# Optimization experiments

Hardware: AMD Instinct MI355X
Metric: run time of the kernel (lower is better)

## Reference

```python
import jax, jax.numpy as jnp
import numpy as np

B, T = 16, 100
MCL = 100      # MAX_CODE_LEN
D_IN = 200     # input_dim (= ques_encoding)
D_BERT = 768
KC = 50        # KC_one_hot_dim
KCD = 100      # kc_embed_dim
HID = 128
SCALE_BERT = 100
TW = 0.5       # QPALA_config.total_attention_weight
BTW = 0.5      # BLAA_config.total_attention_weight


def setup_inputs():
    key = jax.random.key(0)
    ks = jax.random.split(key, 20)
    f32 = jnp.float32
    # composite input feature vector: [ques_enc | code2vec idx | bert | time | score | kc one-hot]
    rnn_first = (jax.random.uniform(ks[0], (B, T, D_IN)) < 0.1).astype(f32)
    c2v = jax.random.randint(ks[1], (B, T, 3 * MCL), 0, 10000).astype(f32)
    bert = jax.random.normal(ks[2], (B, T, D_BERT), f32)
    time_f = jax.random.uniform(ks[3], (B, T, 10), f32)
    score_f = jax.random.uniform(ks[4], (B, T, 2), f32)
    kc = (jax.random.uniform(ks[5], (B, T, KC)) < 0.15).astype(f32)
    x = jnp.concatenate([rnn_first, c2v, bert, time_f, score_f, kc], axis=2)  # [B,T,1330]
    s = 0.05
    p = lambda k, shp: jax.random.normal(k, shp, f32) * s
    return dict(
        x=x,
        node_emb=p(ks[6], (10002, 100)),
        path_emb=p(ks[7], (20002, 100)),
        Wb=p(ks[8], (SCALE_BERT, D_BERT)), bb=jnp.zeros((SCALE_BERT,), f32),
        Wna=p(ks[9], (500, 500)), bna=jnp.zeros((500,), f32),
        Wia=p(ks[10], (KCD, 500)), bia=jnp.zeros((KCD,), f32),
        Wattn=p(ks[11], (1, 500)), battn=jnp.zeros((1,), f32),
        kc_emb=p(ks[12], (KC, KCD)),
        Wt=p(ks[13], (1, SCALE_BERT + KC + KCD)), bt=jnp.zeros((1,), f32),
        Wih=p(ks[14], (4 * HID, 950)), Whh=p(ks[15], (4 * HID, HID)),
        bih=jnp.zeros((4 * HID,), f32), bhh=jnp.zeros((4 * HID,), f32),
        Wfc=p(ks[16], (100, HID + KC + D_IN)), bfc=jnp.zeros((100,), f32),
    )


def _lstm(xseq, Wih, Whh, bih, bhh):
    # PyTorch LSTM, gate order i,f,g,o; batch_first
    bsz = xseq.shape[0]
    pre = jnp.einsum('btd,gd->btg', xseq, Wih) + bih + bhh  # [B,T,4H]

    def step(carry, g_in):
        h, c = carry
        g = g_in + h @ Whh.T
        i, f, gg, o = jnp.split(g, 4, axis=-1)
        c = jax.nn.sigmoid(f) * c + jax.nn.sigmoid(i) * jnp.tanh(gg)
        h = jax.nn.sigmoid(o) * jnp.tanh(c)
        return (h, c), h

    init = (jnp.zeros((bsz, HID), xseq.dtype), jnp.zeros((bsz, HID), xseq.dtype))
    _, hs = jax.lax.scan(step, init, jnp.swapaxes(pre, 0, 1))
    return jnp.swapaxes(hs, 0, 1)


def _forward(x, node_emb, path_emb, Wb, bb, Wna, bna, Wia, bia, Wattn, battn,
             kc_emb, Wt, bt, Wih, Whh, bih, bhh, Wfc, bfc):
    b, t = x.shape[0], x.shape[1]
    rnn_first = x[:, :, :D_IN]
    bert = x[:, :, 500:500 + D_BERT]
    kc_part = x[:, :, 1280:1280 + KC]
    c2v = x[:, :, D_IN:D_IN + 3 * MCL].reshape(b, t, MCL, 3).astype(jnp.int32)
    # gather embeddings + broadcast encoding -> full_embed [B,T,MCL,500]
    full = jnp.concatenate([
        node_emb[c2v[..., 0]], node_emb[c2v[..., 2]], path_emb[c2v[..., 1]],
        jnp.broadcast_to(rnn_first[:, :, None, :], (b, t, MCL, D_IN))], axis=3)
    bert_vec = bert @ Wb.T + bb  # [B,T,100]
    # non-interactive attention pooling (NB: original softmaxes over dim=1 = time)
    cw = jnp.tanh(full @ Wna.T + bna) @ Wattn.T + battn  # [B,T,MCL,1]
    aw = jax.nn.softmax(cw, axis=1)
    na = jnp.sum(full * aw, axis=2)  # [B,T,500]
    kcn = jnp.sum(kc_part, axis=2, keepdims=True)
    kcn = jnp.where(kcn == 0, 1.0, kcn)
    # interactive (KC) cross attention
    trans = full @ Wia.T + bia  # [B,T,MCL,KCD]
    Q = kc_part[..., None] * kc_emb[None, None]  # [B,T,KC,KCD]
    attn = jax.nn.softmax(jnp.einsum('btkd,btmd->btkm', Q, trans), axis=-1)
    Hm = jnp.einsum('btkm,btmd->btkd', attn, trans) * kc_part[..., None]
    ia = jnp.sum(Hm, axis=2) / kcn  # [B,T,KCD]
    rnn_input = jnp.concatenate([kc_part, rnn_first, ia, na, bert_vec], axis=2)  # [B,T,950]
    lstm_out = _lstm(rnn_input, Wih, Whh, bih, bhh)  # [B,T,HID]
    # per-time-step causal attention over lstm_out (vectorized form of the python loop)
    w = (jnp.concatenate([bert_vec, kc_part, ia], axis=2) @ Wt.T + bt)[..., 0]  # [B,T]
    mask = jnp.tril(jnp.ones((t, t), bool))
    logits = jnp.where(mask[None], w[:, None, :], -1e30)
    cattn = jax.nn.softmax(logits, axis=-1)  # [B,T,T]
    cur = jnp.einsum('bij,bjh->bih', cattn, lstm_out)
    attended = lstm_out * (1.0 - TW)
    attended = attended.at[:, 0].set(lstm_out[:, 0])
    idx = jnp.arange(t)
    addm = ((idx >= 1) & (idx <= t - 2)).astype(x.dtype)[None, :, None]
    attended = attended + cur * BTW * addm
    out = jax.nn.sigmoid(
        jnp.concatenate([rnn_first, kc_part, attended], axis=2) @ Wfc.T + bfc)
    return out  # [B,T,100]


def reference(x, node_emb, path_emb, Wb, bb, Wna, bna, Wia, bia, Wattn, battn,
              kc_emb, Wt, bt, Wih, Whh, bih, bhh, Wfc, bfc):
    return _forward(x, node_emb, path_emb, Wb, bb, Wna, bna, Wia, bia, Wattn, battn,
                    kc_emb, Wt, bt, Wih, Whh, bih, bhh, Wfc, bfc)
```

## Files before the change

kernel.cpp:

```cpp
#include <hip/hip_runtime.h>
#include <math.h>

typedef unsigned short ushort_t;
typedef __attribute__((ext_vector_type(8))) short bf16x8;
typedef __attribute__((ext_vector_type(4))) float f32x4;

constexpr int CB = 16, CT = 100, CMCL = 100, CDIN = 200;
constexpr int CKC = 50, CHID = 128;
constexpr int XCH = 1330;
constexpr int NBT = CB * CT;
constexpr int NNODE = 10002, NPATH = 20002;
constexpr int TRS = 114;
constexpr int HSTR = 136;
constexpr int NODE_W = 1536;
constexpr int PATH_W = 768;
constexpr int XR_W   = 640;

__device__ __forceinline__ float frcp(float v){ return __builtin_amdgcn_rcpf(v); }
__device__ __forceinline__ float fsigmoid(float v){ return frcp(1.f + __expf(-v)); }
__device__ __forceinline__ float ftanh_(float v){
  float e = __expf(-2.f*fabsf(v));
  return copysignf((1.f - e) * frcp(1.f + e), v);
}
__device__ __forceinline__ float wredsum(float v){
  #pragma unroll
  for (int off = 32; off; off >>= 1) v += __shfl_xor(v, off);
  return v;
}
__device__ __forceinline__ float wredmax(float v){
  #pragma unroll
  for (int off = 32; off; off >>= 1) v = fmaxf(v, __shfl_xor(v, off));
  return v;
}
__device__ __forceinline__ ushort_t f2b(float f){
  union { float f; unsigned u; } c{f};
  return (ushort_t)((c.u + 0x7FFFu + ((c.u >> 16) & 1u)) >> 16);
}
__device__ __forceinline__ float b2f(unsigned hbits){
  union { unsigned u; float f; } c{hbits << 16};
  return c.f;
}
__device__ __forceinline__ void b8f(const ushort_t* p, float* o){
  uint4 v = *reinterpret_cast<const uint4*>(p);
  o[0]=b2f(v.x & 0xFFFFu); o[1]=b2f(v.x >> 16);
  o[2]=b2f(v.y & 0xFFFFu); o[3]=b2f(v.y >> 16);
  o[4]=b2f(v.z & 0xFFFFu); o[5]=b2f(v.z >> 16);
  o[6]=b2f(v.w & 0xFFFFu); o[7]=b2f(v.w >> 16);
}

struct GDesc {
  const float* A; const float* B; float* Cf; ushort_t* Cb;
  int lda, kOff, kMax, K, M, Npad, rbp, cb, nsplit, ldc, blocks;
};
struct MegaArgs { GDesc d[4]; int nd; };

__global__ __launch_bounds__(256) void mega_gemm(MegaArgs args)
{
  constexpr int KS = 136;
  __shared__ ushort_t As[128*KS];
  __shared__ ushort_t Bs[128*KS];
  int id = blockIdx.x;
  int di = 0;
  while (di < args.nd-1 && id >= args.d[di].blocks) { id -= args.d[di].blocks; ++di; }
  GDesc g = args.d[di];
  const int per = g.rbp * g.cb;
  const int sp = id / per, r = id % per;
  const int xcd = r & 7, s2 = r >> 3;
  const int y = xcd + 8*(s2 / g.cb), cbi = s2 % g.cb;
  const int bm = y*128, bn = cbi*128;
  if (bm >= g.M) return;
  const int tid = threadIdx.x, lane = tid & 63, w = tid >> 6;
  const int wm = w & 1, wn = w >> 1;
  const int lr = lane & 15, lkq = lane >> 4;
  const int kbase = g.kOff + sp * g.K;
  const int hK = g.K >> 1;

  for (int f = tid; f < 128*hK; f += 256) {
    int row = f / hK, j2 = (f % hK)*2;
    int gm = bm + row;
    float2 va = make_float2(0.f,0.f);
    if (gm < g.M && kbase + j2 + 2 <= g.kMax)
      va = *reinterpret_cast<const float2*>(g.A + (long)gm*g.lda + kbase + j2);
    *reinterpret_cast<unsigned*>(&As[row*KS + j2]) = (unsigned)f2b(va.x) | ((unsigned)f2b(va.y)<<16);
    float2 vb = *reinterpret_cast<const float2*>(g.B + ((long)sp*g.Npad + bn + row)*g.K + j2);
    *reinterpret_cast<unsigned*>(&Bs[row*KS + j2]) = (unsigned)f2b(vb.x) | ((unsigned)f2b(vb.y)<<16);
  }
  const int padw = (128 - g.K) >> 1;
  for (int f = tid; f < 128*padw; f += 256) {
    int row = f / padw, jd = f % padw;
    *reinterpret_cast<unsigned*>(&As[row*KS + g.K + jd*2]) = 0u;
    *reinterpret_cast<unsigned*>(&Bs[row*KS + g.K + jd*2]) = 0u;
  }
  __syncthreads();

  f32x4 acc[4][4];
  #pragma unroll
  for (int i = 0; i < 4; ++i)
    #pragma unroll
    for (int j = 0; j < 4; ++j) acc[i][j] = f32x4{0.f,0.f,0.f,0.f};
  #pragma unroll
  for (int ks = 0; ks < 4; ++ks) {
    const int ko = ks*32 + lkq*8;
    bf16x8 af[4], bf[4];
    #pragma unroll
    for (int i = 0; i < 4; ++i)
      af[i] = *reinterpret_cast<const bf16x8*>(&As[(wm*64 + i*16 + lr)*KS + ko]);
    #pragma unroll
    for (int j = 0; j < 4; ++j)
      bf[j] = *reinterpret_cast<const bf16x8*>(&Bs[(wn*64 + j*16 + lr)*KS + ko]);
    #pragma unroll
    for (int i = 0; i < 4; ++i)
      #pragma unroll
      for (int j = 0; j < 4; ++j)
        acc[i][j] = __builtin_amdgcn_mfma_f32_16x16x32_bf16(af[i], bf[j], acc[i][j], 0, 0, 0);
  }
  #pragma unroll
  for (int i = 0; i < 4; ++i) {
    #pragma unroll
    for (int j = 0; j < 4; ++j) {
      #pragma unroll
      for (int rr = 0; rr < 4; ++rr) {
        int gr = bm + wm*64 + i*16 + lkq*4 + rr;
        int gc = bn + wn*64 + j*16 + lr;
        if (gr < g.M) {
          if (g.Cb) g.Cb[(long)gr * g.ldc + gc] = f2b(acc[i][j][rr]);
          else      g.Cf[((long)sp*g.M + gr)*g.ldc + gc] = acc[i][j][rr];
        }
      }
    }
  }
}

constexpr long PK_E0 = (long)NODE_W*100;
constexpr long PK_E1 = PK_E0 + (long)PATH_W*100;
constexpr long PK_E2 = PK_E1 + 2L*XR_W*100;
constexpr long PK_E3 = PK_E2 + 6L*128*128;
constexpr long PK_E4 = PK_E3 + 10L*512*96;
constexpr long PK_E5 = PK_E4 + 512;
constexpr long PK_E6 = PK_E5 + 378L*100;

__global__ void pack_all(
    const float* __restrict__ Wna, const float* __restrict__ Wia,
    const float* __restrict__ bna, const float* __restrict__ bia,
    const float* __restrict__ Wb, const float* __restrict__ Wih,
    const float* __restrict__ Wattn, const float* __restrict__ Wfc,
    float* __restrict__ Bn, float* __restrict__ Bp,
    float* __restrict__ XB2, float* __restrict__ bias_x,
    float* __restrict__ BertB, float* __restrict__ P2B,
    ushort_t* __restrict__ WAB, float* __restrict__ WfcT)
{
  long i = (long)blockIdx.x*256 + threadIdx.x;
  if (i < PK_E0) {
    int n = (int)(i / 100), k = (int)(i % 100);
    float v = 0.f;
    if (n < 500)                      v = Wna[(long)n*500 + k];
    else if (n >= 512 && n < 1012)    v = Wna[(long)(n-512)*500 + 100 + k];
    else if (n >= 1024 && n < 1124)   v = (k == n-1024) ? 1.f : 0.f;
    else if (n >= 1136 && n < 1236)   v = Wia[(long)(n-1136)*500 + k];
    else if (n >= 1280 && n < 1380)   v = (k == n-1280) ? 1.f : 0.f;
    else if (n >= 1392 && n < 1492)   v = Wia[(long)(n-1392)*500 + 100 + k];
    Bn[i] = v;
  } else if (i < PK_E1) {
    long j = i - PK_E0;
    int n = (int)(j / 100), k = (int)(j % 100);
    float v = 0.f;
    if (n < 500)                    v = Wna[(long)n*500 + 200 + k];
    else if (n >= 512 && n < 612)   v = (k == n-512) ? 1.f : 0.f;
    else if (n >= 624 && n < 724)   v = Wia[(long)(n-624)*500 + 200 + k];
    Bp[j] = v;
  } else if (i < PK_E2) {
    long j = i - PK_E1;
    if (j < XR_W) {
      float b = 0.f;
      if (j < 500) b = bna[j];
      else if (j >= 512 && j < 612) b = bia[j-512];
      bias_x[j] = b;
    }
    int s = (int)(j / (XR_W*100)), n = (int)((j / 100) % XR_W), k = (int)(j % 100);
    int k2 = s*100 + k;
    float v = 0.f;
    if (n < 500)                  v = Wna[(long)n*500 + 300 + k2];
    else if (n >= 512 && n < 612) v = Wia[(long)(n-512)*500 + 300 + k2];
    XB2[j] = v;
  } else if (i < PK_E3) {
    long j = i - PK_E2;
    int s = (int)(j / (128*128)), n = (int)((j / 128) % 128), k = (int)(j % 128);
    BertB[j] = (n < 100) ? Wb[(long)n*768 + s*128 + k] : 0.f;
  } else if (i < PK_E4) {
    long j = i - PK_E3;
    int s = (int)(j / (512*96)), n = (int)((j / 96) % 512), k = (int)(j % 96);
    int kg = s*96 + k;
    P2B[j] = (kg < 950) ? Wih[(long)n*950 + kg] : 0.f;
  } else if (i < PK_E5) {
    long j = i - PK_E4;
    WAB[j] = (j < 500) ? f2b(Wattn[j]) : (ushort_t)0;
  } else if (i < PK_E6) {
    long j = i - PK_E5;
    int o = (int)(j / 378), q = (int)(j % 378);
    WfcT[q*100 + o] = Wfc[j];
  }
}

__global__ __launch_bounds__(256) void reduce1(
    const float* __restrict__ xrP, const float* __restrict__ bias_x, ushort_t* __restrict__ XR,
    const float* __restrict__ bertP, const float* __restrict__ bb, float* __restrict__ rnn)
{
  int bt = blockIdx.x, tid = threadIdx.x;
  for (int c = tid; c < XR_W; c += 256) {
    float v = xrP[(long)bt*XR_W + c] + xrP[((long)NBT + bt)*XR_W + c] + bias_x[c];
    XR[(long)bt*XR_W + c] = f2b(v);
  }
  if (tid < 100) {
    float v = bb[tid];
    #pragma unroll
    for (int s = 0; s < 6; ++s) v += bertP[((long)s*NBT + bt)*128 + tid];
    rnn[(long)bt*950 + 850 + tid] = v;
  }
}

__global__ __launch_bounds__(512) void reduce_p2(
    const float* __restrict__ p2P, const float* __restrict__ bih, const float* __restrict__ bhh,
    ushort_t* __restrict__ P2)
{
  int bt = blockIdx.x, g = threadIdx.x;
  float v = bih[g] + bhh[g];
  #pragma unroll
  for (int s = 0; s < 10; ++s) v += p2P[((long)s*NBT + bt)*512 + g];
  int bq = bt / CT, tt = bt % CT;
  int q = g >> 7, rem = g & 127, ww = rem >> 4, lr2 = rem & 15;
  int lk2 = bq >> 2, rr = bq & 3;
  P2[((((long)tt*4 + q)*8 + ww)*4 + lk2)*64 + lr2*4 + rr] = f2b(v);
}

__global__ __launch_bounds__(256) void cw2_kernel(
    const float* __restrict__ x, const ushort_t* __restrict__ NODE_ALL,
    const ushort_t* __restrict__ PATH_ALL, const ushort_t* __restrict__ XR,
    const ushort_t* __restrict__ WAB,
    const float* __restrict__ battn, float* __restrict__ cwT)
{
  int bt = blockIdx.x, b = bt / CT, t = bt % CT;
  int tid = threadIdx.x, w = tid >> 6, lane = tid & 63;
  __shared__ int idx_s[300];
  for (int i = tid; i < 300; i += 256) idx_s[i] = (int)x[(long)bt*XCH + 200 + i];
  float rseg[8], wseg[8];
  b8f(XR + (long)bt*XR_W + lane*8, rseg);
  b8f(WAB + lane*8, wseg);
  __syncthreads();
  float bat = battn[0];

  uint4 A0, C0, P0, A1, C1, P1;
  auto issue = [&](int m, uint4& A, uint4& C, uint4& P){
    if (m < CMCL) {
      int ai = idx_s[3*m], pi = idx_s[3*m+1], ci = idx_s[3*m+2];
      A = *reinterpret_cast<const uint4*>(NODE_ALL + (long)ai*NODE_W + lane*8);
      C = *reinterpret_cast<const uint4*>(NODE_ALL + (long)ci*NODE_W + 512 + lane*8);
      P = *reinterpret_cast<const uint4*>(PATH_ALL + (long)pi*PATH_W + lane*8);
    }
  };
  auto proc = [&](int m, const uint4& A, const uint4& C, const uint4& P){
    if (m >= CMCL) return;
    const unsigned ua[4] = {A.x, A.y, A.z, A.w};
    const unsigned uc[4] = {C.x, C.y, C.z, C.w};
    const unsigned up[4] = {P.x, P.y, P.z, P.w};
    float acc = 0.f;
    #pragma unroll
    for (int jj = 0; jj < 4; ++jj) {
      float lo = b2f(ua[jj] & 0xffffu) + b2f(uc[jj] & 0xffffu) + b2f(up[jj] & 0xffffu) + rseg[2*jj];
      float hi = b2f(ua[jj] >> 16)     + b2f(uc[jj] >> 16)     + b2f(up[jj] >> 16)     + rseg[2*jj+1];
      acc = fmaf(ftanh_(lo), wseg[2*jj], acc);
      acc = fmaf(ftanh_(hi), wseg[2*jj+1], acc);
    }
    acc = wredsum(acc);
    if (lane == 0) cwT[((long)b*CMCL + m)*CT + t] = acc + bat;
  };

  issue(w, A0, C0, P0);
  for (int it = 0; it < 25; it += 2) {
    int m0 = w + it*4;
    issue(m0 + 4, A1, C1, P1);
    proc(m0, A0, C0, P0);
    issue(m0 + 8, A0, C0, P0);
    proc(m0 + 4, A1, C1, P1);
  }
}

__global__ void aw_kernel(const float* __restrict__ cwT, float* __restrict__ awT)
{
  int bm = blockIdx.x; int lane = threadIdx.x;
  const float* row = cwT + (long)bm * CT;
  bool h1 = lane < (CT - 64);
  float v0 = row[lane];
  float v1 = h1 ? row[64 + lane] : -3.0e38f;
  float mx = wredmax(fmaxf(v0, v1));
  float e0 = __expf(v0 - mx);
  float e1 = h1 ? __expf(v1 - mx) : 0.f;
  float s = wredsum(e0 + e1);
  float inv = frcp(s);
  awT[(long)bm*CT + lane] = e0 * inv;
  if (h1) awT[(long)bm*CT + 64 + lane] = e1 * inv;
}

__global__ __launch_bounds__(256) void fuse2_kernel(
    const float* __restrict__ x,
    const ushort_t* __restrict__ NODE_ALL, const ushort_t* __restrict__ PATH_ALL,
    const ushort_t* __restrict__ XR, const float* __restrict__ awT,
    const float* __restrict__ kc_emb, float* __restrict__ rnn,
    const float* __restrict__ Wt, const float* __restrict__ bt0, float* __restrict__ wbuf)
{
  int bt = blockIdx.x, b = bt / CT, t = bt % CT;
  int tid = threadIdx.x, w = tid >> 6, lane = tid & 63;
  int sub = lane >> 5, li = lane & 31;

  __shared__ ushort_t tr_s[100*TRS];
  __shared__ float nacc[4][344];
  __shared__ float ia_red[4][104];
  __shared__ float ia_f[100];
  __shared__ float aw_s[100];
  __shared__ int   idx_s[300];
  __shared__ float kcl[CKC];
  __shared__ int   act_k[CKC];
  __shared__ int   nact_s;
  __shared__ float kcn_s, awsum_s;

  for (int i = tid; i < 300; i += 256) idx_s[i] = (int)x[(long)bt*XCH + 200 + i];
  if (tid < 100) aw_s[tid] = awT[((long)b*CMCL + tid)*CT + t];
  if (tid < CKC) kcl[tid] = x[(long)bt*XCH + 1280 + tid];
  __syncthreads();
  if (tid == 0) {
    float kcn = 0.f; int na = 0;
    for (int k = 0; k < CKC; ++k) { float v = kcl[k]; kcn += v; if (v != 0.f) act_k[na++] = k; }
    nact_s = na; kcn_s = (kcn == 0.f) ? 1.f : kcn;
    float s = 0.f;
    for (int m = 0; m < CMCL; ++m) s += aw_s[m];
    awsum_s = s;
  }
  float rwseg[8];
  if (li >= 14 && li < 28) b8f(XR + (long)bt*XR_W + 512 + (li-14)*8, rwseg);
  __syncthreads();

  float na_a[8] = {}, na_c[8] = {}, na_p[8] = {};
  uint4 A0, C0, P0, A1, C1, P1;
  auto g_issue = [&](int m, uint4& A, uint4& C, uint4& P){
    if (m < CMCL) {
      int ai = idx_s[3*m], pi = idx_s[3*m+1], ci = idx_s[3*m+2];
      A = *reinterpret_cast<const uint4*>(NODE_ALL + (long)ai*NODE_W + 1024 + li*8);
      C = *reinterpret_cast<const uint4*>(NODE_ALL + (long)ci*NODE_W + 1280 + li*8);
      P = *reinterpret_cast<const uint4*>(PATH_ALL + (long)pi*PATH_W + 512  + li*8);
    }
  };
  auto g_proc = [&](int m, const uint4& A, const uint4& C, const uint4& P){
    if (m >= CMCL || li >= 28) return;
    const unsigned ua[4] = {A.x, A.y, A.z, A.w};
    const unsigned uc[4] = {C.x, C.y, C.z, C.w};
    const unsigned up[4] = {P.x, P.y, P.z, P.w};
    if (li < 14) {
      float awm = aw_s[m];
      #pragma unroll
      for (int jj = 0; jj < 4; ++jj) {
        na_a[2*jj]   = fmaf(awm, b2f(ua[jj] & 0xffffu), na_a[2*jj]);
        na_a[2*jj+1] = fmaf(awm, b2f(ua[jj] >> 16),     na_a[2*jj+1]);
        na_c[2*jj]   = fmaf(awm, b2f(uc[jj] & 0xffffu), na_c[2*jj]);
        na_c[2*jj+1] = fmaf(awm, b2f(uc[jj] >> 16),     na_c[2*jj+1]);
        na_p[2*jj]   = fmaf(awm, b2f(up[jj] & 0xffffu), na_p[2*jj]);
        na_p[2*jj+1] = fmaf(awm, b2f(up[jj] >> 16),     na_p[2*jj+1]);
      }
    } else {
      unsigned* d32 = reinterpret_cast<unsigned*>(&tr_s[m*TRS + (li-14)*8]);
      #pragma unroll
      for (int jj = 0; jj < 4; ++jj) {
        float lo = b2f(ua[jj] & 0xffffu) + b2f(uc[jj] & 0xffffu) + b2f(up[jj] & 0xffffu) + rwseg[2*jj];
        float hi = b2f(ua[jj] >> 16)     + b2f(uc[jj] >> 16)     + b2f(up[jj] >> 16)     + rwseg[2*jj+1];
        d32[jj] = (unsigned)f2b(lo) | ((unsigned)f2b(hi) << 16);
      }
    }
  };
  const int mb = w*2 + sub;
  g_issue(mb, A0, C0, P0);
  for (int it = 0; it < 13; it += 2) {
    g_issue((it+1)*8 + mb, A1, C1, P1);
    g_proc(it*8 + mb, A0, C0, P0);
    g_issue((it+2)*8 + mb, A0, C0, P0);
    g_proc((it+1)*8 + mb, A1, C1, P1);
  }
  #pragma unroll
  for (int j = 0; j < 8; ++j) {
    na_a[j] += __shfl_xor(na_a[j], 32);
    na_c[j] += __shfl_xor(na_c[j], 32);
    na_p[j] += __shfl_xor(na_p[j], 32);
  }
  if (lane < 14) {
    #pragma unroll
    for (int j = 0; j < 8; ++j) {
      nacc[w][      lane*8 + j] = na_a[j];
      nacc[w][112 + lane*8 + j] = na_c[j];
      nacc[w][224 + lane*8 + j] = na_p[j];
    }
  }
  __syncthreads();

  for (int q = tid; q < 336; q += 256) {
    float v = nacc[0][q] + nacc[1][q] + nacc[2][q] + nacc[3][q];
    int seg = q / 112, col = q % 112;
    if (col < 100) rnn[(long)bt*950 + 350 + seg*100 + col] = v;
  }
  for (int q = tid; q < CDIN; q += 256) {
    float xv = x[(long)bt*XCH + q];
    rnn[(long)bt*950 + 50 + q] = xv;
    rnn[(long)bt*950 + 650 + q] = awsum_s * xv;
  }
  if (tid < CKC) rnn[(long)bt*950 + tid] = kcl[tid];

  float ia0 = 0.f, ia1 = 0.f;
  const bool vrow1 = lane < 36;
  const bool vpv   = lane < 50;
  const int nact = nact_s;
  const unsigned* tr32_0 = reinterpret_cast<const unsigned*>(&tr_s[lane*TRS]);
  const unsigned* tr32_1 = reinterpret_cast<const unsigned*>(&tr_s[(64+lane)*TRS]);
  const unsigned* tr32   = reinterpret_cast<const unsigned*>(tr_s);
  for (int ki = w; ki < nact; ki += 4) {
    int k = act_k[ki];
    float kck = kcl[k];
    const float* ke = kc_emb + (long)k*100;
    float s0 = 0.f, s1 = 0.f;
    #pragma unroll 5
    for (int dh = 0; dh < 50; ++dh) {
      float k0 = ke[2*dh], k1 = ke[2*dh+1];
      unsigned u0 = tr32_0[dh];
      s0 = fmaf(k0, b2f(u0 & 0xffffu), s0);
      s0 = fmaf(k1, b2f(u0 >> 16), s0);
      if (vrow1) {
        unsigned u1 = tr32_1[dh];
        s1 = fmaf(k0, b2f(u1 & 0xffffu), s1);
        s1 = fmaf(k1, b2f(u1 >> 16), s1);
      }
    }
    s0 *= kck; s1 *= kck;
    float mx = wredmax(fmaxf(s0, vrow1 ? s1 : -3.0e38f));
    float p0e = __expf(s0 - mx);
    float p1e = vrow1 ? __expf(s1 - mx) : 0.f;
    float sm = wredsum(p0e + p1e);
    float inv = kck * frcp(sm);
    p0e *= inv; p1e *= inv;
    #pragma unroll 4
    for (int m = 0; m < CMCL; ++m) {
      float pm = (m < 64) ? __shfl(p0e, m) : __shfl(p1e, m - 64);
      if (vpv) {
        unsigned u = tr32[m*57 + lane];
        ia0 = fmaf(pm, b2f(u & 0xffffu), ia0);
        ia1 = fmaf(pm, b2f(u >> 16), ia1);
      }
    }
  }
  if (vpv) { ia_red[w][2*lane] = ia0; ia_red[w][2*lane+1] = ia1; }
  __syncthreads();
  if (tid < 100) {
    float v = (ia_red[0][tid] + ia_red[1][tid] + ia_red[2][tid] + ia_red[3][tid]) * frcp(kcn_s);
    rnn[(long)bt*950 + 250 + tid] = v;
    ia_f[tid] = v;
  }
  __syncthreads();
  if (tid < 64) {
    float acc = 0.f;
    for (int i = tid; i < 250; i += 64) {
      float f;
      if (i < 100)      f = rnn[(long)bt*950 + 850 + i];
      else if (i < 150) f = kcl[i - 100];
      else              f = ia_f[i - 150];
      acc = fmaf(Wt[i], f, acc);
    }
    acc = wredsum(acc);
    if (tid == 0) wbuf[bt] = acc + bt0[0];
  }
}

__global__ __launch_bounds__(512) void lstm_mfma2(
    const ushort_t* __restrict__ P2,
    const float* __restrict__ Whh,
    float* __restrict__ lstm_out)
{
  const int tid = threadIdx.x, lane = tid & 63, w = tid >> 6;
  const int lr = lane & 15, lkq = lane >> 4;
  __shared__ ushort_t H[2][16 * HSTR];
  {
    ushort_t* hp = &H[0][0];
    for (int i = tid; i < 2*16*HSTR; i += 512) hp[i] = 0;
  }

  bf16x8 bw0[4], bw1[4], bw2[4], bw3[4];
  #pragma unroll
  for (int kk = 0; kk < 4; ++kk) {
    short s[8];
    const float* wp0 = Whh + (long)(0*128 + w*16 + lr) * 128 + kk*32 + lkq*8;
    const float* wp1 = Whh + (long)(1*128 + w*16 + lr) * 128 + kk*32 + lkq*8;
    const float* wp2 = Whh + (long)(2*128 + w*16 + lr) * 128 + kk*32 + lkq*8;
    const float* wp3 = Whh + (long)(3*128 + w*16 + lr) * 128 + kk*32 + lkq*8;
    #pragma unroll
    for (int j = 0; j < 8; ++j) s[j] = (short)f2b(wp0[j]);
    bw0[kk] = bf16x8{s[0],s[1],s[2],s[3],s[4],s[5],s[6],s[7]};
    #pragma unroll
    for (int j = 0; j < 8; ++j) s[j] = (short)f2b(wp1[j]);
    bw1[kk] = bf16x8{s[0],s[1],s[2],s[3],s[4],s[5],s[6],s[7]};
    #pragma unroll
    for (int j = 0; j < 8; ++j) s[j] = (short)f2b(wp2[j]);
    bw2[kk] = bf16x8{s[0],s[1],s[2],s[3],s[4],s[5],s[6],s[7]};
    #pragma unroll
    for (int j = 0; j < 8; ++j) s[j] = (short)f2b(wp3[j]);
    bw3[kk] = bf16x8{s[0],s[1],s[2],s[3],s[4],s[5],s[6],s[7]};
  }

  auto pptr = [&](int t, int q){
    return reinterpret_cast<const uint2*>(P2 + (((((long)t*4 + q)*8 + w)*4 + lkq)*64 + lr*4));
  };
  uint2 pc0 = *pptr(0,0), pc1 = *pptr(0,1), pc2 = *pptr(0,2), pc3 = *pptr(0,3);
  uint2 pn0, pn1, pn2, pn3;
  f32x4 c = {0.f,0.f,0.f,0.f};
  __syncthreads();

  int pb = 0;
  for (int t = 0; t < CT; ++t) {
    if (t + 1 < CT) { pn0 = *pptr(t+1,0); pn1 = *pptr(t+1,1); pn2 = *pptr(t+1,2); pn3 = *pptr(t+1,3); }
    bf16x8 a[4];
    #pragma unroll
    for (int kk = 0; kk < 4; ++kk)
      a[kk] = *reinterpret_cast<const bf16x8*>(&H[pb][lr*HSTR + kk*32 + lkq*8]);
    f32x4 acc0 = f32x4{ b2f(pc0.x & 0xffffu), b2f(pc0.x >> 16), b2f(pc0.y & 0xffffu), b2f(pc0.y >> 16) };
    f32x4 acc1 = f32x4{ b2f(pc1.x & 0xffffu), b2f(pc1.x >> 16), b2f(pc1.y & 0xffffu), b2f(pc1.y >> 16) };
    f32x4 acc2 = f32x4{ b2f(pc2.x & 0xffffu), b2f(pc2.x >> 16), b2f(pc2.y & 0xffffu), b2f(pc2.y >> 16) };
    f32x4 acc3 = f32x4{ b2f(pc3.x & 0xffffu), b2f(pc3.x >> 16), b2f(pc3.y & 0xffffu), b2f(pc3.y >> 16) };
    #pragma unroll
    for (int kk = 0; kk < 4; ++kk) {
      acc0 = __builtin_amdgcn_mfma_f32_16x16x32_bf16(a[kk], bw0[kk], acc0, 0,0,0);
      acc1 = __builtin_amdgcn_mfma_f32_16x16x32_bf16(a[kk], bw1[kk], acc1, 0,0,0);
      acc2 = __builtin_amdgcn_mfma_f32_16x16x32_bf16(a[kk], bw2[kk], acc2, 0,0,0);
      acc3 = __builtin_amdgcn_mfma_f32_16x16x32_bf16(a[kk], bw3[kk], acc3, 0,0,0);
    }
    #pragma unroll
    for (int r = 0; r < 4; ++r) {
      float ig = fsigmoid(acc0[r]);
      float fg = fsigmoid(acc1[r]);
      float gg = ftanh_(acc2[r]);
      float og = fsigmoid(acc3[r]);
      c[r] = fg*c[r] + ig*gg;
      float h = og * ftanh_(c[r]);
      int row = lkq*4 + r;
      H[pb^1][row*HSTR + w*16 + lr] = f2b(h);
      lstm_out[((long)row*CT + t)*128 + w*16 + lr] = h;
    }
    __syncthreads();
    pb ^= 1;
    pc0 = pn0; pc1 = pn1; pc2 = pn2; pc3 = pn3;
  }
}

__global__ __launch_bounds__(256) void final_kernel(
    const float* __restrict__ x, const float* __restrict__ wbuf,
    const float* __restrict__ lstm_out, const float* __restrict__ WfcT,
    const float* __restrict__ bfc, float* __restrict__ out)
{
  int bt = blockIdx.x; int b = bt / CT, i = bt % CT;
  int tid = threadIdx.x;
  __shared__ float p_s[CT];
  __shared__ float feat_s[384];
  if (tid < 64) {
    bool h1 = (64 + tid) < CT;
    float v0 = (tid <= i) ? wbuf[(long)b*CT + tid] : -3.0e38f;
    float v1 = (h1 && (64 + tid) <= i) ? wbuf[(long)b*CT + 64 + tid] : -3.0e38f;
    float mx = wredmax(fmaxf(v0, v1));
    float e0 = (tid <= i) ? __expf(v0 - mx) : 0.f;
    float e1 = (h1 && (64 + tid) <= i) ? __expf(v1 - mx) : 0.f;
    float s = wredsum(e0 + e1);
    float inv = frcp(s);
    p_s[tid] = e0 * inv;
    if (h1) p_s[64 + tid] = e1 * inv;
  }
  __syncthreads();
  if (tid < CHID) {
    float cur = 0.f;
    #pragma unroll 4
    for (int j = 0; j <= i; ++j) cur = fmaf(p_s[j], lstm_out[((long)b*CT + j)*CHID + tid], cur);
    float l = lstm_out[((long)b*CT + i)*CHID + tid];
    float att;
    if (i == 0) att = l;
    else { att = 0.5f * l; if (i <= CT - 2) att = fmaf(0.5f, cur, att); }
    feat_s[250 + tid] = att;
  }
  for (int q = tid; q < 250; q += 256)
    feat_s[q] = (q < 200) ? x[(long)bt*XCH + q] : x[(long)bt*XCH + 1280 + (q - 200)];
  __syncthreads();
  if (tid < 100) {
    float acc = bfc[tid];
    #pragma unroll 4
    for (int q = 0; q < 378; ++q) acc = fmaf(WfcT[q*100 + tid], feat_s[q], acc);
    out[(long)bt*100 + tid] = fsigmoid(acc);
  }
}

extern "C" void kernel_launch(void* const* d_in, const int* in_sizes, int n_in,
                              void* d_out, int out_size, void* d_ws, size_t ws_size,
                              hipStream_t stream) {
  (void)in_sizes; (void)n_in; (void)out_size; (void)ws_size;
  const float* x        = (const float*)d_in[0];
  const float* node_emb = (const float*)d_in[1];
  const float* path_emb = (const float*)d_in[2];
  const float* Wb       = (const float*)d_in[3];
  const float* bb       = (const float*)d_in[4];
  const float* Wna      = (const float*)d_in[5];
  const float* bna      = (const float*)d_in[6];
  const float* Wia      = (const float*)d_in[7];
  const float* bia      = (const float*)d_in[8];
  const float* Wattn    = (const float*)d_in[9];
  const float* battn    = (const float*)d_in[10];
  const float* kc_emb   = (const float*)d_in[11];
  const float* Wt       = (const float*)d_in[12];
  const float* bt0      = (const float*)d_in[13];
  const float* Wih      = (const float*)d_in[14];
  const float* Whh      = (const float*)d_in[15];
  const float* bih      = (const float*)d_in[16];
  const float* bhh      = (const float*)d_in[17];
  const float* Wfc      = (const float*)d_in[18];
  const float* bfc      = (const float*)d_in[19];
  float* out = (float*)d_out;

  char* cur = (char*)d_ws;
  auto alloc = [&](size_t bytes)->char* {
    char* p = cur; cur += (bytes + 255) & ~(size_t)255; return p;
  };
  ushort_t* NODE_ALL = (ushort_t*)alloc((size_t)NNODE*NODE_W*2);
  ushort_t* PATH_ALL = (ushort_t*)alloc((size_t)NPATH*PATH_W*2);
  ushort_t* XR   = (ushort_t*)alloc((size_t)NBT*XR_W*2);
  float* Bn     = (float*)alloc((size_t)NODE_W*100*4);
  float* Bp     = (float*)alloc((size_t)PATH_W*100*4);
  float* XB2    = (float*)alloc((size_t)2*XR_W*100*4);
  float* BertB  = (float*)alloc((size_t)6*128*128*4);
  float* P2B    = (float*)alloc((size_t)10*512*96*4);
  float* bias_x = (float*)alloc((size_t)XR_W*4);
  ushort_t* WAB = (ushort_t*)alloc(512*2);
  float* cwT  = (float*)alloc((size_t)NBT*100*4);
  float* awT  = (float*)alloc((size_t)NBT*100*4);
  float* rnn  = (float*)alloc((size_t)NBT*950*4);
  char*  uni  = alloc((size_t)10*NBT*512*4);
  float* xrP   = (float*)uni;
  float* bertP = (float*)(uni + (size_t)2*NBT*XR_W*4);
  float* p2P   = (float*)uni;
  ushort_t* P2 = (ushort_t*)alloc((size_t)NBT*512*2);
  float* lstm = (float*)alloc((size_t)NBT*128*4);
  float* wbuf = (float*)alloc((size_t)NBT*4);
  float* WfcT = (float*)alloc((size_t)378*100*4);

  pack_all<<<(unsigned)((PK_E6 + 255)/256), 256, 0, stream>>>(
      Wna, Wia, bna, bia, Wb, Wih, Wattn, Wfc,
      Bn, Bp, XB2, bias_x, BertB, P2B, WAB, WfcT);

  {
    MegaArgs a{};
    a.nd = 4;
    a.d[0] = { node_emb, Bn, nullptr, NODE_ALL, 100, 0, 100, 100, NNODE, NODE_W, 80, 12, 1, NODE_W, 80*12 };
    a.d[1] = { path_emb, Bp, nullptr, PATH_ALL, 100, 0, 100, 100, NPATH, PATH_W, 160, 6, 1, PATH_W, 160*6 };
    a.d[2] = { x, BertB, bertP, nullptr, XCH, 500, 1268, 128, NBT, 128, 16, 1, 6, 128, 16*1*6 };
    a.d[3] = { x, XB2, xrP, nullptr, XCH, 0, 200, 100, NBT, XR_W, 16, 5, 2, XR_W, 16*5*2 };
    int total = a.d[0].blocks + a.d[1].blocks + a.d[2].blocks + a.d[3].blocks;
    mega_gemm<<<total, 256, 0, stream>>>(a);
  }
  reduce1<<<NBT, 256, 0, stream>>>(xrP, bias_x, XR, bertP, bb, rnn);

  cw2_kernel<<<NBT,256,0,stream>>>(x, NODE_ALL, PATH_ALL, XR, WAB, battn, cwT);
  aw_kernel<<<CB*CMCL,64,0,stream>>>(cwT, awT);
  fuse2_kernel<<<NBT,256,0,stream>>>(x, NODE_ALL, PATH_ALL, XR, awT, kc_emb, rnn, Wt, bt0, wbuf);

  {
    MegaArgs a{};
    a.nd = 1;
    a.d[0] = { rnn, P2B, p2P, nullptr, 950, 0, 950, 96, NBT, 512, 16, 4, 10, 512, 16*4*10 };
    mega_gemm<<<a.d[0].blocks, 256, 0, stream>>>(a);
  }
  reduce_p2<<<NBT, 512, 0, stream>>>(p2P, bih, bhh, P2);

  lstm_mfma2<<<1,512,0,stream>>>(P2, Whh, lstm);
  final_kernel<<<NBT,256,0,stream>>>(x, wbuf, lstm, WfcT, bfc, out);
}
```

Measured before the change: 485.7 us.

## Store attention-path projected embeddings in custom FP8 and widen fuse2 to 512 threads

Splits the projected node/path embedding tables into an 8-bit (software e4m3-like) table used by the attention-score kernel and a bf16 table used by the fusion kernel. The XR row projection is split the same way. This halves the gather bytes in cw2_kernel at the cost of extra decode ALU work and lower precision inside the tanh attention logits. fuse2_kernel moves to 512 threads with 8 warps sharing the per-code gather loop and reductions, to add parallelism.

```diff
diff --git a/kernel.cpp b/kernel.cpp
--- a/kernel.cpp
+++ b/kernel.cpp
@@ -2,6 +2,7 @@
 #include <math.h>
 
 typedef unsigned short ushort_t;
+typedef unsigned char uchar_t;
 typedef __attribute__((ext_vector_type(8))) short bf16x8;
 typedef __attribute__((ext_vector_type(4))) float f32x4;
 
@@ -12,9 +13,11 @@
 constexpr int NNODE = 10002, NPATH = 20002;
 constexpr int TRS = 114;
 constexpr int HSTR = 136;
-constexpr int NODE_W = 1536;
-constexpr int PATH_W = 768;
-constexpr int XR_W   = 640;
+constexpr int NT8_W = 1024;
+constexpr int NTB_W = 512;
+constexpr int PT8_W = 512;
+constexpr int PTB_W = 256;
+constexpr int XR_W  = 640;
 
 __device__ __forceinline__ float frcp(float v){ return __builtin_amdgcn_rcpf(v); }
 __device__ __forceinline__ float fsigmoid(float v){ return frcp(1.f + __expf(-v)); }
@@ -47,12 +50,41 @@
   o[4]=b2f(v.z & 0xFFFFu); o[5]=b2f(v.z >> 16);
   o[6]=b2f(v.w & 0xFFFFu); o[7]=b2f(v.w >> 16);
 }
+__device__ __forceinline__ uchar_t ff8(float f){
+  union { float f; unsigned u; } c{f};
+  unsigned s = (c.u >> 24) & 0x80u;
+  c.u &= 0x7FFFFFFFu;
+  float a = c.f;
+  unsigned b;
+  if (a < 0.015625f) {
+    b = (unsigned)(a * 512.f + 0.5f);
+  } else {
+    unsigned u = c.u + (0x0007FFFFu + ((c.u >> 20) & 1u));
+    int e = (int)(u >> 23) - 120;
+    unsigned mm = (u >> 20) & 7u;
+    if (e >= 16) { e = 15; mm = 6; }
+    b = ((unsigned)e << 3) | mm;
+  }
+  return (uchar_t)(s | b);
+}
+__device__ __forceinline__ float f8d(unsigned b){
+  unsigned e = (b >> 3) & 15u, m = b & 7u;
+  union { unsigned u; float f; } c{((e + 120u) << 23) | (m << 20)};
+  float v = e ? c.f : (float)m * 0.001953125f;
+  return (b & 0x80u) ? -v : v;
+}
+__device__ __forceinline__ void f8x8(uint2 p, float* o){
+  #pragma unroll
+  for (int j = 0; j < 4; ++j) o[j]     = f8d((p.x >> (8*j)) & 255u);
+  #pragma unroll
+  for (int j = 0; j < 4; ++j) o[4 + j] = f8d((p.y >> (8*j)) & 255u);
+}
 
 struct GDesc {
-  const float* A; const float* B; float* Cf; ushort_t* Cb;
-  int lda, kOff, kMax, K, M, Npad, rbp, cb, nsplit, ldc, blocks;
+  const float* A; const float* B; float* Cf; void* Cb;
+  int lda, kOff, kMax, K, M, Npad, rbp, cb, nsplit, ldc, omode, blocks;
 };
-struct MegaArgs { GDesc d[4]; int nd; };
+struct MegaArgs { GDesc d[6]; int nd; };
 
 __global__ __launch_bounds__(256) void mega_gemm(MegaArgs args)
 {
@@ -123,28 +155,33 @@
         int gr = bm + wm*64 + i*16 + lkq*4 + rr;
         int gc = bn + wn*64 + j*16 + lr;
         if (gr < g.M) {
-          if (g.Cb) g.Cb[(long)gr * g.ldc + gc] = f2b(acc[i][j][rr]);
-          else      g.Cf[((long)sp*g.M + gr)*g.ldc + gc] = acc[i][j][rr];
+          float v = acc[i][j][rr];
+          if (g.omode == 2)      ((uchar_t*)g.Cb)[(long)gr * g.ldc + gc] = ff8(v);
+          else if (g.omode == 1) ((ushort_t*)g.Cb)[(long)gr * g.ldc + gc] = f2b(v);
+          else                   g.Cf[((long)sp*g.M + gr)*g.ldc + gc] = v;
         }
       }
     }
   }
 }
 
-constexpr long PK_E0 = (long)NODE_W*100;
-constexpr long PK_E1 = PK_E0 + (long)PATH_W*100;
-constexpr long PK_E2 = PK_E1 + 2L*XR_W*100;
-constexpr long PK_E3 = PK_E2 + 6L*128*128;
-constexpr long PK_E4 = PK_E3 + 10L*512*96;
-constexpr long PK_E5 = PK_E4 + 512;
-constexpr long PK_E6 = PK_E5 + 378L*100;
+constexpr long PK_E0 = 1024L*100;
+constexpr long PK_E1 = PK_E0 + 512L*100;
+constexpr long PK_E2 = PK_E1 + 512L*100;
+constexpr long PK_E3 = PK_E2 + 256L*100;
+constexpr long PK_E4 = PK_E3 + 2L*XR_W*100;
+constexpr long PK_E5 = PK_E4 + 6L*128*128;
+constexpr long PK_E6 = PK_E5 + 10L*512*96;
+constexpr long PK_E7 = PK_E6 + 512;
+constexpr long PK_E8 = PK_E7 + 378L*100;
 
 __global__ void pack_all(
     const float* __restrict__ Wna, const float* __restrict__ Wia,
     const float* __restrict__ bna, const float* __restrict__ bia,
     const float* __restrict__ Wb, const float* __restrict__ Wih,
     const float* __restrict__ Wattn, const float* __restrict__ Wfc,
-    float* __restrict__ Bn, float* __restrict__ Bp,
+    float* __restrict__ Bn8, float* __restrict__ Bnb,
+    float* __restrict__ Bp8, float* __restrict__ Bpb,
     float* __restrict__ XB2, float* __restrict__ bias_x,
     float* __restrict__ BertB, float* __restrict__ P2B,
     ushort_t* __restrict__ WAB, float* __restrict__ WfcT)
@@ -153,23 +190,31 @@
   if (i < PK_E0) {
     int n = (int)(i / 100), k = (int)(i % 100);
     float v = 0.f;
-    if (n < 500)                      v = Wna[(long)n*500 + k];
-    else if (n >= 512 && n < 1012)    v = Wna[(long)(n-512)*500 + 100 + k];
-    else if (n >= 1024 && n < 1124)   v = (k == n-1024) ? 1.f : 0.f;
-    else if (n >= 1136 && n < 1236)   v = Wia[(long)(n-1136)*500 + k];
-    else if (n >= 1280 && n < 1380)   v = (k == n-1280) ? 1.f : 0.f;
-    else if (n >= 1392 && n < 1492)   v = Wia[(long)(n-1392)*500 + 100 + k];
-    Bn[i] = v;
+    if (n < 500)                    v = Wna[(long)n*500 + k];
+    else if (n >= 512 && n < 1012)  v = Wna[(long)(n-512)*500 + 100 + k];
+    Bn8[i] = v;
   } else if (i < PK_E1) {
     long j = i - PK_E0;
     int n = (int)(j / 100), k = (int)(j % 100);
     float v = 0.f;
-    if (n < 500)                    v = Wna[(long)n*500 + 200 + k];
-    else if (n >= 512 && n < 612)   v = (k == n-512) ? 1.f : 0.f;
-    else if (n >= 624 && n < 724)   v = Wia[(long)(n-624)*500 + 200 + k];
-    Bp[j] = v;
+    if (n < 100)                    v = (k == n) ? 1.f : 0.f;
+    else if (n >= 112 && n < 212)   v = Wia[(long)(n-112)*500 + k];
+    else if (n >= 256 && n < 356)   v = (k == n-256) ? 1.f : 0.f;
+    else if (n >= 368 && n < 468)   v = Wia[(long)(n-368)*500 + 100 + k];
+    Bnb[j] = v;
   } else if (i < PK_E2) {
     long j = i - PK_E1;
+    int n = (int)(j / 100), k = (int)(j % 100);
+    Bp8[j] = (n < 500) ? Wna[(long)n*500 + 200 + k] : 0.f;
+  } else if (i < PK_E3) {
+    long j = i - PK_E2;
+    int n = (int)(j / 100), k = (int)(j % 100);
+    float v = 0.f;
+    if (n < 100)                    v = (k == n) ? 1.f : 0.f;
+    else if (n >= 112 && n < 212)   v = Wia[(long)(n-112)*500 + 200 + k];
+    Bpb[j] = v;
+  } else if (i < PK_E4) {
+    long j = i - PK_E3;
     if (j < XR_W) {
       float b = 0.f;
       if (j < 500) b = bna[j];
@@ -182,33 +227,35 @@
     if (n < 500)                  v = Wna[(long)n*500 + 300 + k2];
     else if (n >= 512 && n < 612) v = Wia[(long)(n-512)*500 + 300 + k2];
     XB2[j] = v;
-  } else if (i < PK_E3) {
-    long j = i - PK_E2;
+  } else if (i < PK_E5) {
+    long j = i - PK_E4;
     int s = (int)(j / (128*128)), n = (int)((j / 128) % 128), k = (int)(j % 128);
     BertB[j] = (n < 100) ? Wb[(long)n*768 + s*128 + k] : 0.f;
-  } else if (i < PK_E4) {
-    long j = i - PK_E3;
+  } else if (i < PK_E6) {
+    long j = i - PK_E5;
     int s = (int)(j / (512*96)), n = (int)((j / 96) % 512), k = (int)(j % 96);
     int kg = s*96 + k;
     P2B[j] = (kg < 950) ? Wih[(long)n*950 + kg] : 0.f;
-  } else if (i < PK_E5) {
-    long j = i - PK_E4;
+  } else if (i < PK_E7) {
+    long j = i - PK_E6;
     WAB[j] = (j < 500) ? f2b(Wattn[j]) : (ushort_t)0;
-  } else if (i < PK_E6) {
-    long j = i - PK_E5;
+  } else if (i < PK_E8) {
+    long j = i - PK_E7;
     int o = (int)(j / 378), q = (int)(j % 378);
     WfcT[q*100 + o] = Wfc[j];
   }
 }
 
 __global__ __launch_bounds__(256) void reduce1(
-    const float* __restrict__ xrP, const float* __restrict__ bias_x, ushort_t* __restrict__ XR,
+    const float* __restrict__ xrP, const float* __restrict__ bias_x,
+    uchar_t* __restrict__ XRF8, ushort_t* __restrict__ XRBF,
     const float* __restrict__ bertP, const float* __restrict__ bb, float* __restrict__ rnn)
 {
   int bt = blockIdx.x, tid = threadIdx.x;
   for (int c = tid; c < XR_W; c += 256) {
     float v = xrP[(long)bt*XR_W + c] + xrP[((long)NBT + bt)*XR_W + c] + bias_x[c];
-    XR[(long)bt*XR_W + c] = f2b(v);
+    if (c < 512) XRF8[(long)bt*512 + c] = ff8(v);
+    else         XRBF[(long)bt*128 + (c - 512)] = f2b(v);
   }
   if (tid < 100) {
     float v = bb[tid];
@@ -233,8 +280,8 @@
 }
 
 __global__ __launch_bounds__(256) void cw2_kernel(
-    const float* __restrict__ x, const ushort_t* __restrict__ NODE_ALL,
-    const ushort_t* __restrict__ PATH_ALL, const ushort_t* __restrict__ XR,
+    const float* __restrict__ x, const uchar_t* __restrict__ NT8,
+    const uchar_t* __restrict__ PT8, const uchar_t* __restrict__ XRF8,
     const ushort_t* __restrict__ WAB,
     const float* __restrict__ battn, float* __restrict__ cwT)
 {
@@ -243,33 +290,28 @@
   __shared__ int idx_s[300];
   for (int i = tid; i < 300; i += 256) idx_s[i] = (int)x[(long)bt*XCH + 200 + i];
   float rseg[8], wseg[8];
-  b8f(XR + (long)bt*XR_W + lane*8, rseg);
+  f8x8(*reinterpret_cast<const uint2*>(XRF8 + (long)bt*512 + lane*8), rseg);
   b8f(WAB + lane*8, wseg);
   __syncthreads();
   float bat = battn[0];
 
-  uint4 A0, C0, P0, A1, C1, P1;
-  auto issue = [&](int m, uint4& A, uint4& C, uint4& P){
+  uint2 A0, C0, P0, A1, C1, P1;
+  auto issue = [&](int m, uint2& A, uint2& C, uint2& P){
     if (m < CMCL) {
       int ai = idx_s[3*m], pi = idx_s[3*m+1], ci = idx_s[3*m+2];
-      A = *reinterpret_cast<const uint4*>(NODE_ALL + (long)ai*NODE_W + lane*8);
-      C = *reinterpret_cast<const uint4*>(NODE_ALL + (long)ci*NODE_W + 512 + lane*8);
-      P = *reinterpret_cast<const uint4*>(PATH_ALL + (long)pi*PATH_W + lane*8);
+      A = *reinterpret_cast<const uint2*>(NT8 + (long)ai*NT8_W + lane*8);
+      C = *reinterpret_cast<const uint2*>(NT8 + (long)ci*NT8_W + 512 + lane*8);
+      P = *reinterpret_cast<const uint2*>(PT8 + (long)pi*PT8_W + lane*8);
     }
   };
-  auto proc = [&](int m, const uint4& A, const uint4& C, const uint4& P){
+  auto proc = [&](int m, const uint2& A, const uint2& C, const uint2& P){
     if (m >= CMCL) return;
-    const unsigned ua[4] = {A.x, A.y, A.z, A.w};
-    const unsigned uc[4] = {C.x, C.y, C.z, C.w};
-    const unsigned up[4] = {P.x, P.y, P.z, P.w};
+    float fa[8], fc[8], fp[8];
+    f8x8(A, fa); f8x8(C, fc); f8x8(P, fp);
     float acc = 0.f;
     #pragma unroll
-    for (int jj = 0; jj < 4; ++jj) {
-      float lo = b2f(ua[jj] & 0xffffu) + b2f(uc[jj] & 0xffffu) + b2f(up[jj] & 0xffffu) + rseg[2*jj];
-      float hi = b2f(ua[jj] >> 16)     + b2f(uc[jj] >> 16)     + b2f(up[jj] >> 16)     + rseg[2*jj+1];
-      acc = fmaf(ftanh_(lo), wseg[2*jj], acc);
-      acc = fmaf(ftanh_(hi), wseg[2*jj+1], acc);
-    }
+    for (int j = 0; j < 8; ++j)
+      acc = fmaf(ftanh_(fa[j] + fc[j] + fp[j] + rseg[j]), wseg[j], acc);
     acc = wredsum(acc);
     if (lane == 0) cwT[((long)b*CMCL + m)*CT + t] = acc + bat;
   };
@@ -300,10 +342,10 @@
   if (h1) awT[(long)bm*CT + 64 + lane] = e1 * inv;
 }
 
-__global__ __launch_bounds__(256) void fuse2_kernel(
+__global__ __launch_bounds__(512) void fuse2_kernel(
     const float* __restrict__ x,
-    const ushort_t* __restrict__ NODE_ALL, const ushort_t* __restrict__ PATH_ALL,
-    const ushort_t* __restrict__ XR, const float* __restrict__ awT,
+    const ushort_t* __restrict__ NTB, const ushort_t* __restrict__ PTB,
+    const ushort_t* __restrict__ XRBF, const float* __restrict__ awT,
     const float* __restrict__ kc_emb, float* __restrict__ rnn,
     const float* __restrict__ Wt, const float* __restrict__ bt0, float* __restrict__ wbuf)
 {
@@ -312,8 +354,8 @@
   int sub = lane >> 5, li = lane & 31;
 
   __shared__ ushort_t tr_s[100*TRS];
-  __shared__ float nacc[4][344];
-  __shared__ float ia_red[4][104];
+  __shared__ float nacc[8][344];
+  __shared__ float ia_red[8][104];
   __shared__ float ia_f[100];
   __shared__ float aw_s[100];
   __shared__ int   idx_s[300];
@@ -322,7 +364,7 @@
   __shared__ int   nact_s;
   __shared__ float kcn_s, awsum_s;
 
-  for (int i = tid; i < 300; i += 256) idx_s[i] = (int)x[(long)bt*XCH + 200 + i];
+  for (int i = tid; i < 300; i += 512) idx_s[i] = (int)x[(long)bt*XCH + 200 + i];
   if (tid < 100) aw_s[tid] = awT[((long)b*CMCL + tid)*CT + t];
   if (tid < CKC) kcl[tid] = x[(long)bt*XCH + 1280 + tid];
   __syncthreads();
@@ -335,21 +377,22 @@
     awsum_s = s;
   }
   float rwseg[8];
-  if (li >= 14 && li < 28) b8f(XR + (long)bt*XR_W + 512 + (li-14)*8, rwseg);
+  if (li >= 14 && li < 28) b8f(XRBF + (long)bt*128 + (li-14)*8, rwseg);
   __syncthreads();
 
   float na_a[8] = {}, na_c[8] = {}, na_p[8] = {};
+  const bool gv = (li < 28);
   uint4 A0, C0, P0, A1, C1, P1;
   auto g_issue = [&](int m, uint4& A, uint4& C, uint4& P){
-    if (m < CMCL) {
+    if (m < CMCL && gv) {
       int ai = idx_s[3*m], pi = idx_s[3*m+1], ci = idx_s[3*m+2];
-      A = *reinterpret_cast<const uint4*>(NODE_ALL + (long)ai*NODE_W + 1024 + li*8);
-      C = *reinterpret_cast<const uint4*>(NODE_ALL + (long)ci*NODE_W + 1280 + li*8);
-      P = *reinterpret_cast<const uint4*>(PATH_ALL + (long)pi*PATH_W + 512  + li*8);
+      A = *reinterpret_cast<const uint4*>(NTB + (long)ai*NTB_W + li*8);
+      C = *reinterpret_cast<const uint4*>(NTB + (long)ci*NTB_W + 256 + li*8);
+      P = *reinterpret_cast<const uint4*>(PTB + (long)pi*PTB_W + li*8);
     }
   };
   auto g_proc = [&](int m, const uint4& A, const uint4& C, const uint4& P){
-    if (m >= CMCL || li >= 28) return;
+    if (m >= CMCL || !gv) return;
     const unsigned ua[4] = {A.x, A.y, A.z, A.w};
     const unsigned uc[4] = {C.x, C.y, C.z, C.w};
     const unsigned up[4] = {P.x, P.y, P.z, P.w};
@@ -376,11 +419,11 @@
   };
   const int mb = w*2 + sub;
   g_issue(mb, A0, C0, P0);
-  for (int it = 0; it < 13; it += 2) {
-    g_issue((it+1)*8 + mb, A1, C1, P1);
-    g_proc(it*8 + mb, A0, C0, P0);
-    g_issue((it+2)*8 + mb, A0, C0, P0);
-    g_proc((it+1)*8 + mb, A1, C1, P1);
+  for (int it = 0; it < 8; it += 2) {
+    g_issue((it+1)*16 + mb, A1, C1, P1);
+    g_proc(it*16 + mb, A0, C0, P0);
+    g_issue((it+2)*16 + mb, A0, C0, P0);
+    g_proc((it+1)*16 + mb, A1, C1, P1);
   }
   #pragma unroll
   for (int j = 0; j < 8; ++j) {
@@ -398,12 +441,14 @@
   }
   __syncthreads();
 
-  for (int q = tid; q < 336; q += 256) {
-    float v = nacc[0][q] + nacc[1][q] + nacc[2][q] + nacc[3][q];
+  for (int q = tid; q < 336; q += 512) {
+    float v = 0.f;
+    #pragma unroll
+    for (int ww2 = 0; ww2 < 8; ++ww2) v += nacc[ww2][q];
     int seg = q / 112, col = q % 112;
     if (col < 100) rnn[(long)bt*950 + 350 + seg*100 + col] = v;
   }
-  for (int q = tid; q < CDIN; q += 256) {
+  for (int q = tid; q < CDIN; q += 512) {
     float xv = x[(long)bt*XCH + q];
     rnn[(long)bt*950 + 50 + q] = xv;
     rnn[(long)bt*950 + 650 + q] = awsum_s * xv;
@@ -417,7 +462,7 @@
   const unsigned* tr32_0 = reinterpret_cast<const unsigned*>(&tr_s[lane*TRS]);
   const unsigned* tr32_1 = reinterpret_cast<const unsigned*>(&tr_s[(64+lane)*TRS]);
   const unsigned* tr32   = reinterpret_cast<const unsigned*>(tr_s);
-  for (int ki = w; ki < nact; ki += 4) {
+  for (int ki = w; ki < nact; ki += 8) {
     int k = act_k[ki];
     float kck = kcl[k];
     const float* ke = kc_emb + (long)k*100;
@@ -454,7 +499,10 @@
   if (vpv) { ia_red[w][2*lane] = ia0; ia_red[w][2*lane+1] = ia1; }
   __syncthreads();
   if (tid < 100) {
-    float v = (ia_red[0][tid] + ia_red[1][tid] + ia_red[2][tid] + ia_red[3][tid]) * frcp(kcn_s);
+    float v = 0.f;
+    #pragma unroll
+    for (int ww2 = 0; ww2 < 8; ++ww2) v += ia_red[ww2][tid];
+    v *= frcp(kcn_s);
     rnn[(long)bt*950 + 250 + tid] = v;
     ia_f[tid] = v;
   }
@@ -625,11 +673,16 @@
   auto alloc = [&](size_t bytes)->char* {
     char* p = cur; cur += (bytes + 255) & ~(size_t)255; return p;
   };
-  ushort_t* NODE_ALL = (ushort_t*)alloc((size_t)NNODE*NODE_W*2);
-  ushort_t* PATH_ALL = (ushort_t*)alloc((size_t)NPATH*PATH_W*2);
-  ushort_t* XR   = (ushort_t*)alloc((size_t)NBT*XR_W*2);
-  float* Bn     = (float*)alloc((size_t)NODE_W*100*4);
-  float* Bp     = (float*)alloc((size_t)PATH_W*100*4);
+  uchar_t* NT8   = (uchar_t*)alloc((size_t)NNODE*NT8_W);
+  ushort_t* NTB  = (ushort_t*)alloc((size_t)NNODE*NTB_W*2);
+  uchar_t* PT8   = (uchar_t*)alloc((size_t)NPATH*PT8_W);
+  ushort_t* PTB  = (ushort_t*)alloc((size_t)NPATH*PTB_W*2);
+  uchar_t* XRF8  = (uchar_t*)alloc((size_t)NBT*512);
+  ushort_t* XRBF = (ushort_t*)alloc((size_t)NBT*128*2);
+  float* Bn8    = (float*)alloc((size_t)1024*100*4);
+  float* Bnb    = (float*)alloc((size_t)512*100*4);
+  float* Bp8    = (float*)alloc((size_t)512*100*4);
+  float* Bpb    = (float*)alloc((size_t)256*100*4);
   float* XB2    = (float*)alloc((size_t)2*XR_W*100*4);
   float* BertB  = (float*)alloc((size_t)6*128*128*4);
   float* P2B    = (float*)alloc((size_t)10*512*96*4);
@@ -647,30 +700,33 @@
   float* wbuf = (float*)alloc((size_t)NBT*4);
   float* WfcT = (float*)alloc((size_t)378*100*4);
 
-  pack_all<<<(unsigned)((PK_E6 + 255)/256), 256, 0, stream>>>(
+  pack_all<<<(unsigned)((PK_E8 + 255)/256), 256, 0, stream>>>(
       Wna, Wia, bna, bia, Wb, Wih, Wattn, Wfc,
-      Bn, Bp, XB2, bias_x, BertB, P2B, WAB, WfcT);
+      Bn8, Bnb, Bp8, Bpb, XB2, bias_x, BertB, P2B, WAB, WfcT);
 
   {
     MegaArgs a{};
-    a.nd = 4;
-    a.d[0] = { node_emb, Bn, nullptr, NODE_ALL, 100, 0, 100, 100, NNODE, NODE_W, 80, 12, 1, NODE_W, 80*12 };
-    a.d[1] = { path_emb, Bp, nullptr, PATH_ALL, 100, 0, 100, 100, NPATH, PATH_W, 160, 6, 1, PATH_W, 160*6 };
-    a.d[2] = { x, BertB, bertP, nullptr, XCH, 500, 1268, 128, NBT, 128, 16, 1, 6, 128, 16*1*6 };
-    a.d[3] = { x, XB2, xrP, nullptr, XCH, 0, 200, 100, NBT, XR_W, 16, 5, 2, XR_W, 16*5*2 };
-    int total = a.d[0].blocks + a.d[1].blocks + a.d[2].blocks + a.d[3].blocks;
+    a.nd = 6;
+    a.d[0] = { node_emb, Bn8, nullptr, NT8,  100, 0, 100, 100, NNODE, 1024, 80, 8, 1, 1024, 2, 80*8 };
+    a.d[1] = { node_emb, Bnb, nullptr, NTB,  100, 0, 100, 100, NNODE, 512,  80, 4, 1, 512,  1, 80*4 };
+    a.d[2] = { path_emb, Bp8, nullptr, PT8,  100, 0, 100, 100, NPATH, 512, 160, 4, 1, 512,  2, 160*4 };
+    a.d[3] = { path_emb, Bpb, nullptr, PTB,  100, 0, 100, 100, NPATH, 256, 160, 2, 1, 256,  1, 160*2 };
+    a.d[4] = { x, BertB, bertP, nullptr, XCH, 500, 1268, 128, NBT, 128, 16, 1, 6, 128, 0, 16*1*6 };
+    a.d[5] = { x, XB2,   xrP,   nullptr, XCH, 0,   200,  100, NBT, XR_W, 16, 5, 2, XR_W, 0, 16*5*2 };
+    int total = 0;
+    for (int i2 = 0; i2 < 6; ++i2) total += a.d[i2].blocks;
     mega_gemm<<<total, 256, 0, stream>>>(a);
   }
-  reduce1<<<NBT, 256, 0, stream>>>(xrP, bias_x, XR, bertP, bb, rnn);
-
-  cw2_kernel<<<NBT,256,0,stream>>>(x, NODE_ALL, PATH_ALL, XR, WAB, battn, cwT);
+  reduce1<<<NBT, 256, 0, stream>>>(xrP, bias_x, XRF8, XRBF, bertP, bb, rnn);
+
+  cw2_kernel<<<NBT,256,0,stream>>>(x, NT8, PT8, XRF8, WAB, battn, cwT);
   aw_kernel<<<CB*CMCL,64,0,stream>>>(cwT, awT);
-  fuse2_kernel<<<NBT,256,0,stream>>>(x, NODE_ALL, PATH_ALL, XR, awT, kc_emb, rnn, Wt, bt0, wbuf);
+  fuse2_kernel<<<NBT,512,0,stream>>>(x, NTB, PTB, XRBF, awT, kc_emb, rnn, Wt, bt0, wbuf);
 
   {
     MegaArgs a{};
     a.nd = 1;
-    a.d[0] = { rnn, P2B, p2P, nullptr, 950, 0, 950, 96, NBT, 512, 16, 4, 10, 512, 16*4*10 };
+    a.d[0] = { rnn, P2B, p2P, nullptr, 950, 0, 950, 96, NBT, 512, 16, 4, 10, 512, 0, 16*4*10 };
     mega_gemm<<<a.d[0].blocks, 256, 0, stream>>>(a);
   }
   reduce_p2<<<NBT, 512, 0, stream>>>(p2P, bih, bhh, P2);
```

After: 562.6 us. 1.16x slower.
